# Performance work log

Measured on AMD Instinct MI355X. Metric: run time of the kernel, lower is better.

## Reference

```python
import jax, jax.numpy as jnp
import numpy as np

N = 100000
E = 1200000
D_IN = 64
D_OUT = 64
NUM_TYPES = 2


def setup_inputs() -> dict:
    key = jax.random.key(0)
    k1, k2, k3, k4, k5 = jax.random.split(key, 5)
    x = jax.random.normal(k1, (N, D_IN), dtype=jnp.float32)
    W = jax.random.normal(k2, (NUM_TYPES, D_IN, D_OUT), dtype=jnp.float32) / np.sqrt(D_IN)
    b = jax.random.normal(k3, (NUM_TYPES, D_OUT), dtype=jnp.float32) * 0.01
    edge_index = jax.random.randint(k4, (2, E), 0, N, dtype=jnp.int64)
    edge_attr = jax.random.randint(k5, (E,), 0, NUM_TYPES, dtype=jnp.int64)
    return {"x": x, "W": W, "b": b, "edge_index": edge_index, "edge_attr": edge_attr}


def reference(x, W, b, edge_index, edge_attr):
    # PyG flow source_to_target: x_j = x[src], aggregate at dst
    src, dst = edge_index[0], edge_index[1]
    x_j = x[src]                                   # [E, D_IN] gather
    # HeteroLinear with 2 types: compute both small GEMMs, select per edge
    m0 = x_j @ W[0] + b[0]                          # [E, D_OUT]
    m1 = x_j @ W[1] + b[1]                          # [E, D_OUT]
    msg = jnp.where((edge_attr == 0)[:, None], m0, m1)
    # scatter-max aggregation; PyG fills nodes with no incoming edges with 0
    agg = jax.ops.segment_max(msg, dst, num_segments=x.shape[0])
    out = jnp.where(jnp.isneginf(agg), 0.0, agg)
    return out
```

## Files before the change

### kernel.cpp

```cpp
#include <hip/hip_runtime.h>
#include <math.h>

static constexpr int D = 64;
static constexpr int SCAN_BLOCKS = 256;
static constexpr int NB_CHUNK = 96;
static constexpr int BIN_SHIFT = 6;
static constexpr int MAXBINS = 2048;

typedef __bf16 bf16x8 __attribute__((ext_vector_type(8)));
typedef float f32x4 __attribute__((ext_vector_type(4)));


__device__ __forceinline__ unsigned short f2bf(float f) {
  unsigned u = __float_as_uint(f);
  return (unsigned short)((u + 0x7fffu + ((u >> 16) & 1u)) >> 16);
}

__device__ __forceinline__ unsigned short bf_enc(unsigned short u) {
  const unsigned short s = (unsigned short)(-(int)(u >> 15));
  return (unsigned short)(u ^ (s | 0x8000u));
}
__device__ __forceinline__ float bf_dec_to_f32(unsigned enc32) {
  if (enc32 == 0u) return 0.0f;
  unsigned short enc = (unsigned short)(enc32 >> 16);
  unsigned short u = (enc & 0x8000u) ? (unsigned short)(enc ^ 0x8000u)
                                     : (unsigned short)(~enc);
  return __uint_as_float((unsigned)u << 16);
}

__device__ __forceinline__ void atomic_max_float(float* p, float v, float cur) {
  if (!(v > cur)) return;
  if (v >= 0.0f)
    atomicMax(reinterpret_cast<int*>(p), __float_as_int(v));
  else
    atomicMin(reinterpret_cast<unsigned int*>(p), __float_as_uint(v));
}

__global__ void k_init_neginf(float4* __restrict__ out, int n4) {
  int i = blockIdx.x * blockDim.x + threadIdx.x;
  if (i < n4) {
    float4 v;
    v.x = v.y = v.z = v.w = -INFINITY;
    out[i] = v;
  }
}

__global__ __launch_bounds__(256) void k_gemm(
    const float* __restrict__ x, const float* __restrict__ W,
    const float* __restrict__ b, unsigned short* __restrict__ yb, int nN) {
  const int lane = threadIdx.x & 63;
  const int wid = (blockIdx.x << 2) + (threadIdx.x >> 6);
  const int nWaves = gridDim.x << 2;
  const int kgrp = (lane >> 4) << 3;
  const int nsub = lane & 15;

  bf16x8 Bf[8][2];
  float bias[8];
#pragma unroll
  for (int nt = 0; nt < 8; ++nt) {
    const int t = nt >> 2;
    const int n = ((nt & 3) << 4) + nsub;
#pragma unroll
    for (int ks = 0; ks < 2; ++ks) {
      bf16x8 f;
#pragma unroll
      for (int e = 0; e < 8; ++e) {
        const int k = (ks << 5) + kgrp + e;
        f[e] = (__bf16)W[t * 4096 + k * 64 + n];
      }
      Bf[nt][ks] = f;
    }
    bias[nt] = b[t * 64 + n];
  }

  const int nChunks = (nN + 15) >> 4;
  for (int c = wid; c < nChunks; c += nWaves) {
    const int base = c << 4;
    const int arow = min(base + nsub, nN - 1);
    const float4 xa0 = *reinterpret_cast<const float4*>(x + (size_t)arow * 64 + kgrp);
    const float4 xa1 = *reinterpret_cast<const float4*>(x + (size_t)arow * 64 + kgrp + 4);
    const float4 xb0 = *reinterpret_cast<const float4*>(x + (size_t)arow * 64 + 32 + kgrp);
    const float4 xb1 = *reinterpret_cast<const float4*>(x + (size_t)arow * 64 + 36 + kgrp);
    bf16x8 a0, a1;
    a0[0] = (__bf16)xa0.x; a0[1] = (__bf16)xa0.y; a0[2] = (__bf16)xa0.z; a0[3] = (__bf16)xa0.w;
    a0[4] = (__bf16)xa1.x; a0[5] = (__bf16)xa1.y; a0[6] = (__bf16)xa1.z; a0[7] = (__bf16)xa1.w;
    a1[0] = (__bf16)xb0.x; a1[1] = (__bf16)xb0.y; a1[2] = (__bf16)xb0.z; a1[3] = (__bf16)xb0.w;
    a1[4] = (__bf16)xb1.x; a1[5] = (__bf16)xb1.y; a1[6] = (__bf16)xb1.z; a1[7] = (__bf16)xb1.w;
#pragma unroll
    for (int nt = 0; nt < 8; ++nt) {
      f32x4 acc = {bias[nt], bias[nt], bias[nt], bias[nt]};
      acc = __builtin_amdgcn_mfma_f32_16x16x32_bf16(a0, Bf[nt][0], acc, 0, 0, 0);
      acc = __builtin_amdgcn_mfma_f32_16x16x32_bf16(a1, Bf[nt][1], acc, 0, 0, 0);
      const int t = nt >> 2;
      const int o = ((nt & 3) << 4) + nsub;
      const int rbase = base + ((lane >> 4) << 2);
#pragma unroll
      for (int r = 0; r < 4; ++r) {
        const int node = rbase + r;
        if (node < nN)
          yb[((size_t)t * nN + node) * 64 + o] = bf_enc(f2bf(acc[r]));
      }
    }
  }
}


__global__ __launch_bounds__(1024) void k_lochist(const int* __restrict__ dst,
                                                  int* __restrict__ countsT,
                                                  int nE, int nBins, int chunk) {
  __shared__ int lh[MAXBINS];
  const int t = threadIdx.x;
  for (int i = t; i < nBins; i += 1024) lh[i] = 0;
  __syncthreads();
  const int beg = blockIdx.x * chunk;
  const int end = min(beg + chunk, nE);
  for (int i = beg + t; i < end; i += 1024) atomicAdd(&lh[dst[i] >> BIN_SHIFT], 1);
  __syncthreads();
  for (int i = t; i < nBins; i += 1024)
    countsT[(size_t)i * gridDim.x + blockIdx.x] = lh[i];
}

__global__ __launch_bounds__(256) void k_scan_partial(
    const int* __restrict__ counts, int* __restrict__ blockSums, int nN) {
  __shared__ int red[256];
  const int t = threadIdx.x;
  const int seg = (nN + gridDim.x - 1) / gridDim.x;
  const int beg = blockIdx.x * seg;
  const int end = min(beg + seg, nN);
  int s = 0;
  for (int i = beg + t; i < end; i += 256) s += counts[i];
  red[t] = s;
  __syncthreads();
  for (int d = 128; d > 0; d >>= 1) {
    if (t < d) red[t] += red[t + d];
    __syncthreads();
  }
  if (t == 0) blockSums[blockIdx.x] = red[0];
}

__global__ __launch_bounds__(256) void k_scan_write(
    const int* __restrict__ counts, const int* __restrict__ blockSums,
    int* __restrict__ offs, int nN) {
  __shared__ int bs[256];
  __shared__ int sh[256];
  const int t = threadIdx.x;
  bs[t] = blockSums[t];
  __syncthreads();
  for (int d = 1; d < 256; d <<= 1) {
    const int o = (t >= d) ? bs[t - d] : 0;
    __syncthreads();
    bs[t] += o;
    __syncthreads();
  }
  const int bid = blockIdx.x;
  int carry = (bid > 0) ? bs[bid - 1] : 0;
  const int total = bs[255];
  const int seg = (nN + gridDim.x - 1) / gridDim.x;
  const int beg = bid * seg;
  const int end = min(beg + seg, nN);
  for (int base = beg; base < end; base += 256) {
    const int i = base + t;
    const int v = (i < end) ? counts[i] : 0;
    sh[t] = v;
    __syncthreads();
    for (int d = 1; d < 256; d <<= 1) {
      const int o = (t >= d) ? sh[t - d] : 0;
      __syncthreads();
      sh[t] += o;
      __syncthreads();
    }
    if (i < end) offs[i] = carry + sh[t] - v;
    carry += sh[255];
    __syncthreads();
  }
  if (bid == gridDim.x - 1 && t == 0) offs[nN] = total;
}

__global__ __launch_bounds__(1024) void k_cscatter(
    const int* __restrict__ src, const int* __restrict__ dst,
    const int* __restrict__ ea, const int* __restrict__ offs,
    unsigned* __restrict__ rec, int nE, int nBins, int chunk) {
  __shared__ int cur[MAXBINS];
  const int t = threadIdx.x;
  for (int i = t; i < nBins; i += 1024)
    cur[i] = offs[(size_t)i * gridDim.x + blockIdx.x];
  __syncthreads();
  const int beg = blockIdx.x * chunk;
  const int end = min(beg + chunk, nE);
  for (int i = beg + t; i < end; i += 1024) {
    const int d = dst[i];
    const int pos = atomicAdd(&cur[d >> BIN_SHIFT], 1);
    rec[pos] = (unsigned)src[i] | ((unsigned)ea[i] << 20) |
               ((unsigned)(d & ((1 << BIN_SHIFT) - 1)) << 21);
  }
}

__global__ __launch_bounds__(512) void k_reduce_bin(
    const int* __restrict__ offs, const unsigned* __restrict__ rec,
    const unsigned short* __restrict__ yb, float* __restrict__ out, int nN) {
  __shared__ unsigned acc[64 * 64];
  const int t = threadIdx.x;
#pragma unroll
  for (int i = 0; i < 8; ++i) acc[t + i * 512] = 0u;
  __syncthreads();

  const int bin = blockIdx.x;
  const int beg = offs[bin * NB_CHUNK];
  const int cnt = offs[(bin + 1) * NB_CHUNK] - beg;
  const int w = t >> 6;
  const unsigned lane = t & 63;
  const unsigned nNu = (unsigned)nN;
  const int myBeg = beg + ((cnt * w) >> 3);
  const int myEnd = beg + ((cnt * (w + 1)) >> 3);

  int j = myBeg;
  for (; j + 7 < myEnd; j += 8) {
    unsigned r[8];
    unsigned v[8];
#pragma unroll
    for (int q = 0; q < 8; ++q) r[q] = rec[j + q];
#pragma unroll
    for (int q = 0; q < 8; ++q)
      v[q] = (unsigned)yb[((((r[q] >> 20) & 1u) * nNu + (r[q] & 0xFFFFFu)) << 6) + lane] << 16;
#pragma unroll
    for (int q = 0; q < 8; ++q)
      atomicMax(&acc[(((r[q] >> 21) & 63u) << 6) + lane], v[q]);
  }
  for (; j < myEnd; ++j) {
    const unsigned r0 = rec[j];
    const unsigned v0 =
        (unsigned)yb[((((r0 >> 20) & 1u) * nNu + (r0 & 0xFFFFFu)) << 6) + lane] << 16;
    atomicMax(&acc[(((r0 >> 21) & 63u) << 6) + lane], v0);
  }
  __syncthreads();

  const int nodeBase = bin << 6;
  for (int f = t; f < 64 * 16; f += 512) {
    const int node = nodeBase + (f >> 4);
    if (node < nN) {
      float4 v;
      v.x = bf_dec_to_f32(acc[f * 4 + 0]);
      v.y = bf_dec_to_f32(acc[f * 4 + 1]);
      v.z = bf_dec_to_f32(acc[f * 4 + 2]);
      v.w = bf_dec_to_f32(acc[f * 4 + 3]);
      *reinterpret_cast<float4*>(&out[(size_t)node * 64 + (f & 15) * 4]) = v;
    }
  }
}


__global__ void k_fixup(float4* __restrict__ out, int n4) {
  int i = blockIdx.x * blockDim.x + threadIdx.x;
  if (i < n4) {
    float4 v = out[i];
    if (v.x == -INFINITY) v.x = 0.0f;
    if (v.y == -INFINITY) v.y = 0.0f;
    if (v.z == -INFINITY) v.z = 0.0f;
    if (v.w == -INFINITY) v.w = 0.0f;
    out[i] = v;
  }
}

__global__ __launch_bounds__(256) void k_edge_direct(
    const float* __restrict__ x, const float* __restrict__ W,
    const float* __restrict__ b, const int* __restrict__ ei,
    const int* __restrict__ ea, float* __restrict__ out, int nEdges) {
  __shared__ float Wl[2 * D * D];
  __shared__ float bl[2 * D];
  for (int i = threadIdx.x; i < 2 * D * D; i += 256) Wl[i] = W[i];
  for (int i = threadIdx.x; i < 2 * D; i += 256) bl[i] = b[i];
  __syncthreads();
  const int wave = threadIdx.x >> 6;
  const int lane = threadIdx.x & 63;
  for (int e = blockIdx.x * 4 + wave; e < nEdges; e += gridDim.x * 4) {
    const int src = ei[e];
    const int dst = ei[nEdges + e];
    const int t = ea[e];
    const float xk = x[(size_t)src * D + lane];
    float acc = bl[t * D + lane];
    const float* Wt = &Wl[t * D * D];
#pragma unroll
    for (int k = 0; k < D; ++k)
      acc = fmaf(__shfl(xk, k, 64), Wt[k * D + lane], acc);
    float* p = out + (size_t)dst * D + lane;
    const float cur = *p;
    atomic_max_float(p, acc, cur);
  }
}


extern "C" void kernel_launch(void* const* d_in, const int* in_sizes, int n_in,
                              void* d_out, int out_size, void* d_ws, size_t ws_size,
                              hipStream_t stream) {
  const float* x = (const float*)d_in[0];
  const float* W = (const float*)d_in[1];
  const float* b = (const float*)d_in[2];
  const int* ei = (const int*)d_in[3];
  const int* ea = (const int*)d_in[4];
  float* out = (float*)d_out;

  const int nNodes = in_sizes[0] / D;
  const int nEdges = in_sizes[4];
  const int n4out = (nNodes * D) / 4;
  const int nBins = (nNodes + (1 << BIN_SHIFT) - 1) >> BIN_SHIFT;
  const int nScan = nBins * NB_CHUNK;
  const int chunk = (nEdges + NB_CHUNK - 1) / NB_CHUNK;

  auto rup = [](size_t v) { return (v + 255) & ~(size_t)255; };
  const size_t ybB = (size_t)2 * nNodes * D * sizeof(unsigned short);
  const size_t offYb = 0;
  const size_t offCT = rup(offYb + ybB);
  const size_t offOffs = rup(offCT + (size_t)nScan * sizeof(int));
  const size_t offBS = rup(offOffs + (size_t)(nScan + 1) * sizeof(int));
  const size_t offRec = rup(offBS + (size_t)SCAN_BLOCKS * sizeof(int));
  const size_t need = offRec + (size_t)nEdges * sizeof(unsigned);

  if (ws_size >= need && nNodes < (1 << 20) && nBins <= MAXBINS) {
    char* ws = (char*)d_ws;
    unsigned short* yb = (unsigned short*)(ws + offYb);
    int* countsT = (int*)(ws + offCT);
    int* offs = (int*)(ws + offOffs);
    int* blockSums = (int*)(ws + offBS);
    unsigned* rec = (unsigned*)(ws + offRec);

    const int* srcRow = ei;
    const int* dstRow = ei + nEdges;

    k_lochist<<<NB_CHUNK, 1024, 0, stream>>>(dstRow, countsT, nEdges, nBins, chunk);
    k_scan_partial<<<SCAN_BLOCKS, 256, 0, stream>>>(countsT, blockSums, nScan);
    k_scan_write<<<SCAN_BLOCKS, 256, 0, stream>>>(countsT, blockSums, offs, nScan);
    k_cscatter<<<NB_CHUNK, 1024, 0, stream>>>(srcRow, dstRow, ea, offs, rec,
                                              nEdges, nBins, chunk);
    k_gemm<<<512, 256, 0, stream>>>(x, W, b, yb, nNodes);
    k_reduce_bin<<<nBins, 512, 0, stream>>>(offs, rec, yb, out, nNodes);
  } else {
    k_init_neginf<<<(n4out + 255) / 256, 256, 0, stream>>>((float4*)out, n4out);
    k_edge_direct<<<4096, 256, 0, stream>>>(x, W, b, ei, ea, out, nEdges);
    k_fixup<<<(n4out + 255) / 256, 256, 0, stream>>>((float4*)out, n4out);
  }
}
```

Baseline: 167.1 us.

## Fuse GEMM into histogram kernel, vectorize edge loops, precompute typed row index

Merges the node GEMM and the destination histogram into one launch, with the first blocks doing histogram work and the remaining blocks doing the MFMA GEMM. This removes a kernel launch and lets the two independent stages overlap. The histogram and scatter loops now read int4 vectors, and scatter stores src+type*nN directly so the reduce kernel skips the per-record index math. The reduce kernel also uses readfirstlane to make record values wave-uniform. The vector loads assume chunk boundaries are 16-byte aligned, and the GEMM now runs on fewer, larger blocks.

Result: no change. 167.6 us (+0.3%).

```diff
diff --git a/kernel.cpp b/kernel.cpp
--- a/kernel.cpp
+++ b/kernel.cpp
@@ -4,6 +4,7 @@
 static constexpr int D = 64;
 static constexpr int SCAN_BLOCKS = 256;
 static constexpr int NB_CHUNK = 96;
+static constexpr int GEMM_BLOCKS = 128;
 static constexpr int BIN_SHIFT = 6;
 static constexpr int MAXBINS = 2048;
 
@@ -45,12 +46,37 @@
   }
 }
 
-__global__ __launch_bounds__(256) void k_gemm(
+__global__ __launch_bounds__(1024) void k_gemm_hist(
     const float* __restrict__ x, const float* __restrict__ W,
-    const float* __restrict__ b, unsigned short* __restrict__ yb, int nN) {
-  const int lane = threadIdx.x & 63;
-  const int wid = (blockIdx.x << 2) + (threadIdx.x >> 6);
-  const int nWaves = gridDim.x << 2;
+    const float* __restrict__ b, unsigned short* __restrict__ yb,
+    const int* __restrict__ dst, int* __restrict__ countsT,
+    int nN, int nE, int nBins, int chunk) {
+  __shared__ int lh[MAXBINS];
+  const int t = threadIdx.x;
+
+  if (blockIdx.x < NB_CHUNK) {
+    for (int i = t; i < nBins; i += 1024) lh[i] = 0;
+    __syncthreads();
+    const int beg = blockIdx.x * chunk;
+    const int end = min(beg + chunk, nE);
+    int i = beg + t * 4;
+    for (; i + 3 < end; i += 4096) {
+      const int4 d4 = *reinterpret_cast<const int4*>(dst + i);
+      atomicAdd(&lh[d4.x >> BIN_SHIFT], 1);
+      atomicAdd(&lh[d4.y >> BIN_SHIFT], 1);
+      atomicAdd(&lh[d4.z >> BIN_SHIFT], 1);
+      atomicAdd(&lh[d4.w >> BIN_SHIFT], 1);
+    }
+    for (; i < end; ++i) atomicAdd(&lh[dst[i] >> BIN_SHIFT], 1);
+    __syncthreads();
+    for (int i2 = t; i2 < nBins; i2 += 1024)
+      countsT[(size_t)i2 * NB_CHUNK + blockIdx.x] = lh[i2];
+    return;
+  }
+
+  const int lane = t & 63;
+  const int wid = (blockIdx.x - NB_CHUNK) * 16 + (t >> 6);
+  const int nWaves = GEMM_BLOCKS * 16;
   const int kgrp = (lane >> 4) << 3;
   const int nsub = lane & 15;
 
@@ -58,7 +84,7 @@
   float bias[8];
 #pragma unroll
   for (int nt = 0; nt < 8; ++nt) {
-    const int t = nt >> 2;
+    const int ty = nt >> 2;
     const int n = ((nt & 3) << 4) + nsub;
 #pragma unroll
     for (int ks = 0; ks < 2; ++ks) {
@@ -66,11 +92,11 @@
 #pragma unroll
       for (int e = 0; e < 8; ++e) {
         const int k = (ks << 5) + kgrp + e;
-        f[e] = (__bf16)W[t * 4096 + k * 64 + n];
+        f[e] = (__bf16)W[ty * 4096 + k * 64 + n];
       }
       Bf[nt][ks] = f;
     }
-    bias[nt] = b[t * 64 + n];
+    bias[nt] = b[ty * 64 + n];
   }
 
   const int nChunks = (nN + 15) >> 4;
@@ -91,33 +117,17 @@
       f32x4 acc = {bias[nt], bias[nt], bias[nt], bias[nt]};
       acc = __builtin_amdgcn_mfma_f32_16x16x32_bf16(a0, Bf[nt][0], acc, 0, 0, 0);
       acc = __builtin_amdgcn_mfma_f32_16x16x32_bf16(a1, Bf[nt][1], acc, 0, 0, 0);
-      const int t = nt >> 2;
+      const int ty = nt >> 2;
       const int o = ((nt & 3) << 4) + nsub;
       const int rbase = base + ((lane >> 4) << 2);
 #pragma unroll
       for (int r = 0; r < 4; ++r) {
         const int node = rbase + r;
         if (node < nN)
-          yb[((size_t)t * nN + node) * 64 + o] = bf_enc(f2bf(acc[r]));
+          yb[((size_t)ty * nN + node) * 64 + o] = bf_enc(f2bf(acc[r]));
       }
     }
   }
-}
-
-
-__global__ __launch_bounds__(1024) void k_lochist(const int* __restrict__ dst,
-                                                  int* __restrict__ countsT,
-                                                  int nE, int nBins, int chunk) {
-  __shared__ int lh[MAXBINS];
-  const int t = threadIdx.x;
-  for (int i = t; i < nBins; i += 1024) lh[i] = 0;
-  __syncthreads();
-  const int beg = blockIdx.x * chunk;
-  const int end = min(beg + chunk, nE);
-  for (int i = beg + t; i < end; i += 1024) atomicAdd(&lh[dst[i] >> BIN_SHIFT], 1);
-  __syncthreads();
-  for (int i = t; i < nBins; i += 1024)
-    countsT[(size_t)i * gridDim.x + blockIdx.x] = lh[i];
 }
 
 __global__ __launch_bounds__(256) void k_scan_partial(
@@ -179,18 +189,44 @@
 __global__ __launch_bounds__(1024) void k_cscatter(
     const int* __restrict__ src, const int* __restrict__ dst,
     const int* __restrict__ ea, const int* __restrict__ offs,
-    unsigned* __restrict__ rec, int nE, int nBins, int chunk) {
+    unsigned* __restrict__ rec, int nN, int nE, int nBins, int chunk) {
   __shared__ int cur[MAXBINS];
   const int t = threadIdx.x;
   for (int i = t; i < nBins; i += 1024)
-    cur[i] = offs[(size_t)i * gridDim.x + blockIdx.x];
+    cur[i] = offs[(size_t)i * NB_CHUNK + blockIdx.x];
   __syncthreads();
   const int beg = blockIdx.x * chunk;
   const int end = min(beg + chunk, nE);
-  for (int i = beg + t; i < end; i += 1024) {
+  int i = beg + t * 4;
+  for (; i + 3 < end; i += 4096) {
+    const int4 s4 = *reinterpret_cast<const int4*>(src + i);
+    const int4 d4 = *reinterpret_cast<const int4*>(dst + i);
+    const int4 e4 = *reinterpret_cast<const int4*>(ea + i);
+    {
+      const int pos = atomicAdd(&cur[d4.x >> BIN_SHIFT], 1);
+      rec[pos] = (unsigned)(s4.x + e4.x * nN) |
+                 ((unsigned)(d4.x & ((1 << BIN_SHIFT) - 1)) << 21);
+    }
+    {
+      const int pos = atomicAdd(&cur[d4.y >> BIN_SHIFT], 1);
+      rec[pos] = (unsigned)(s4.y + e4.y * nN) |
+                 ((unsigned)(d4.y & ((1 << BIN_SHIFT) - 1)) << 21);
+    }
+    {
+      const int pos = atomicAdd(&cur[d4.z >> BIN_SHIFT], 1);
+      rec[pos] = (unsigned)(s4.z + e4.z * nN) |
+                 ((unsigned)(d4.z & ((1 << BIN_SHIFT) - 1)) << 21);
+    }
+    {
+      const int pos = atomicAdd(&cur[d4.w >> BIN_SHIFT], 1);
+      rec[pos] = (unsigned)(s4.w + e4.w * nN) |
+                 ((unsigned)(d4.w & ((1 << BIN_SHIFT) - 1)) << 21);
+    }
+  }
+  for (; i < end; ++i) {
     const int d = dst[i];
     const int pos = atomicAdd(&cur[d >> BIN_SHIFT], 1);
-    rec[pos] = (unsigned)src[i] | ((unsigned)ea[i] << 20) |
+    rec[pos] = (unsigned)(src[i] + ea[i] * nN) |
                ((unsigned)(d & ((1 << BIN_SHIFT) - 1)) << 21);
   }
 }
@@ -209,28 +245,27 @@
   const int cnt = offs[(bin + 1) * NB_CHUNK] - beg;
   const int w = t >> 6;
   const unsigned lane = t & 63;
-  const unsigned nNu = (unsigned)nN;
   const int myBeg = beg + ((cnt * w) >> 3);
   const int myEnd = beg + ((cnt * (w + 1)) >> 3);
 
   int j = myBeg;
   for (; j + 7 < myEnd; j += 8) {
     unsigned r[8];
+#pragma unroll
+    for (int q = 0; q < 8; ++q)
+      r[q] = __builtin_amdgcn_readfirstlane(rec[j + q]);
     unsigned v[8];
 #pragma unroll
-    for (int q = 0; q < 8; ++q) r[q] = rec[j + q];
-#pragma unroll
     for (int q = 0; q < 8; ++q)
-      v[q] = (unsigned)yb[((((r[q] >> 20) & 1u) * nNu + (r[q] & 0xFFFFFu)) << 6) + lane] << 16;
+      v[q] = (unsigned)yb[((r[q] & 0x1FFFFFu) << 6) + lane] << 16;
 #pragma unroll
     for (int q = 0; q < 8; ++q)
-      atomicMax(&acc[(((r[q] >> 21) & 63u) << 6) + lane], v[q]);
+      atomicMax(&acc[((r[q] >> 21) << 6) + lane], v[q]);
   }
   for (; j < myEnd; ++j) {
-    const unsigned r0 = rec[j];
-    const unsigned v0 =
-        (unsigned)yb[((((r0 >> 20) & 1u) * nNu + (r0 & 0xFFFFFu)) << 6) + lane] << 16;
-    atomicMax(&acc[(((r0 >> 21) & 63u) << 6) + lane], v0);
+    const unsigned r0 = __builtin_amdgcn_readfirstlane(rec[j]);
+    const unsigned v0 = (unsigned)yb[((r0 & 0x1FFFFFu) << 6) + lane] << 16;
+    atomicMax(&acc[((r0 >> 21) << 6) + lane], v0);
   }
   __syncthreads();
 
@@ -326,12 +361,12 @@
     const int* srcRow = ei;
     const int* dstRow = ei + nEdges;
 
-    k_lochist<<<NB_CHUNK, 1024, 0, stream>>>(dstRow, countsT, nEdges, nBins, chunk);
+    k_gemm_hist<<<NB_CHUNK + GEMM_BLOCKS, 1024, 0, stream>>>(
+        x, W, b, yb, dstRow, countsT, nNodes, nEdges, nBins, chunk);
     k_scan_partial<<<SCAN_BLOCKS, 256, 0, stream>>>(countsT, blockSums, nScan);
     k_scan_write<<<SCAN_BLOCKS, 256, 0, stream>>>(countsT, blockSums, offs, nScan);
     k_cscatter<<<NB_CHUNK, 1024, 0, stream>>>(srcRow, dstRow, ea, offs, rec,
-                                              nEdges, nBins, chunk);
-    k_gemm<<<512, 256, 0, stream>>>(x, W, b, yb, nNodes);
+                                              nNodes, nEdges, nBins, chunk);
     k_reduce_bin<<<nBins, 512, 0, stream>>>(offs, rec, yb, out, nNodes);
   } else {
     k_init_neginf<<<(n4out + 255) / 256, 256, 0, stream>>>((float4*)out, n4out);
```
